# Kernel optimization log

Hardware: AMD Instinct MI355X
Metric: run time of the kernel (lower is better)

The kernel has to match this reference:

```python
import jax, jax.numpy as jnp
import numpy as np

BATCH = 16384
NUM_FEATURES = 1024  # sum(field_dims)
CROSS_DIMS = NUM_FEATURES * (NUM_FEATURES - 1) // 2  # 523776


def setup_inputs() -> dict:
    key = jax.random.key(0)
    kx, kw = jax.random.split(key)
    x = jax.random.uniform(kx, (BATCH, NUM_FEATURES), dtype=jnp.float32)
    # xavier-uniform init of a (cross_dims, 1) parameter: bound = sqrt(6/(fan_in+fan_out))
    bound = float(np.sqrt(6.0 / (CROSS_DIMS + 1)))
    w = jax.random.uniform(kw, (CROSS_DIMS,), dtype=jnp.float32, minval=-bound, maxval=bound)
    return {"x": x, "w": w}


def reference(x, w):
    # POLY2: out_b = sigmoid( sum_{i<j} w_{ij} * x_{b,i} * x_{b,j} )
    # sklearn PolynomialFeatures(interaction_only) emits pairs in combinations
    # (row-major i<j) order, identical to triu_indices(k=1) ordering.
    F = x.shape[1]
    iu, ju = jnp.triu_indices(F, k=1)
    W = jnp.zeros((F, F), dtype=x.dtype).at[iu, ju].set(w)  # [F,F] strictly upper-tri
    # quadratic form without materializing the [B, F*(F-1)/2] pairwise matrix
    out = jnp.einsum('bi,ij,bj->b', x, W, x)  # [B]
    return jax.nn.sigmoid(out.astype(jnp.float32))
```

## Files before the change

kernel.cpp:

```cpp
#include <hip/hip_runtime.h>
#include <hip/hip_bf16.h>

#define F 1024
#define B_ROWS 16384

typedef short v8s __attribute__((ext_vector_type(8)));
typedef float v4f __attribute__((ext_vector_type(4)));
typedef unsigned short v8u __attribute__((ext_vector_type(8)));
typedef unsigned short ushort_t;

__device__ __forceinline__ unsigned short f2bf(float f) {
    unsigned int u = __builtin_bit_cast(unsigned int, f);
    u = (u + 0x7FFFu + ((u >> 16) & 1u)) >> 16;
    return (unsigned short)u;
}

__device__ __forceinline__ void gload_lds16(const ushort_t* g, ushort_t* l) {
    __builtin_amdgcn_global_load_lds(
        (const __attribute__((address_space(1))) unsigned int*)g,
        (__attribute__((address_space(3))) unsigned int*)l,
        16, 0, 0);
}


__global__ __launch_bounds__(256) void prep_kernel(
        const float* __restrict__ w, const float* __restrict__ x,
        ushort_t* __restrict__ Bp, ushort_t* __restrict__ Xp,
        float* __restrict__ acc) {
    const int bid  = blockIdx.x;
    const int tid  = threadIdx.x;
    const int lane = tid & 63;
    const int wave = tid >> 6;
    const int l16  = lane & 15;
    const int quad = lane >> 4;

    if (bid < 64) {
        acc[bid * 256 + tid] = 0.0f;
    } else if (bid < 576) {
        const int c  = (bid - 64) * 4 + wave;
        const int n  = (c >> 5) * 16 + l16;
        const int k0 = (c & 31) * 32 + quad * 8;
        v8u o;
#pragma unroll
        for (int e = 0; e < 8; ++e) {
            const int k = k0 + e;
            float v = 0.0f;
            if (k < n) {
                const int idx = k * (F - 1) - (k * (k - 1)) / 2 + (n - k - 1);
                v = w[idx];
            }
            o[e] = f2bf(v);
        }
        *(v8u*)(Bp + (size_t)c * 512 + lane * 8) = o;
    } else {
        const int c  = (bid - 576) * 4 + wave;
        const int r  = (c >> 5) * 16 + l16;
        const int k0 = (c & 31) * 32 + quad * 8;
        const float* src = x + (size_t)r * F + k0;
        float4 v0 = *(const float4*)(src);
        float4 v1 = *(const float4*)(src + 4);
        v8u o;
        o[0] = f2bf(v0.x); o[1] = f2bf(v0.y); o[2] = f2bf(v0.z); o[3] = f2bf(v0.w);
        o[4] = f2bf(v1.x); o[5] = f2bf(v1.y); o[6] = f2bf(v1.z); o[7] = f2bf(v1.w);
        *(v8u*)(Xp + (size_t)c * 512 + lane * 8) = o;
    }
}

__global__ __launch_bounds__(256, 3) void gemm_kernel(
        const ushort_t* __restrict__ Xp,
        const ushort_t* __restrict__ Bp,
        const float*   __restrict__ Xf,
        float*         __restrict__ rowacc) {
    __shared__ ushort_t Bs[2 * 16 * 512];

    const int f   = blockIdx.x;
    const int xcd = f & 7;
    const int g   = f >> 3;
    const int y   = g & 15;
    const int nt  = 7 - (g >> 4);
    const int blockM = (xcd * 16 + y) * 128;
    const int blockN = nt * 128;
    const int nch    = 2 * (nt + 1);

    const int tid   = threadIdx.x;
    const int lane  = tid & 63;
    const int wave  = tid >> 6;
    const int waveM = wave >> 1;
    const int waveN = wave & 1;
    const int quad  = lane >> 4;
    const int l16   = lane & 15;

    const int mg = (blockM >> 4) + waveM * 4;
    const v8s* A8 = (const v8s*)Xp + (size_t)mg * 32 * 64 + lane;

    const int q0   = wave * 4;
    const int ngB  = nt * 8;

#define STAGE_B(c, buf)                                                        \
    {                                                                          \
        _Pragma("unroll")                                                      \
        for (int q = 0; q < 4; ++q) {                                          \
            const int qq  = q0 + q;                                            \
            const int kgl = qq >> 3, ngl = qq & 7;                             \
            gload_lds16(Bp + (size_t)((ngB + ngl) * 32 + (c) * 2 + kgl) * 512 + lane * 8, \
                        Bs + (buf) * 8192 + (kgl * 8 + ngl) * 512);            \
        }                                                                      \
    }

    v4f acc[4][4];
#pragma unroll
    for (int i = 0; i < 4; i++)
#pragma unroll
        for (int j = 0; j < 4; j++) acc[i][j] = (v4f)(0.0f);

    v8s a0[4], a1[4], bfr[4];

    STAGE_B(0, 0)
#pragma unroll
    for (int mi = 0; mi < 4; ++mi) a0[mi] = A8[(mi * 32 + 0) * 64];
    __syncthreads();

    for (int c = 0; c < nch; ++c) {
        const int  buf  = c & 1;
        const bool more = (c + 1 < nch);
        if (more) STAGE_B(c + 1, buf ^ 1)

#pragma unroll
        for (int ni = 0; ni < 4; ++ni)
            bfr[ni] = *(const v8s*)(Bs + buf * 8192 + (0 * 8 + waveN * 4 + ni) * 512 + lane * 8);
#pragma unroll
        for (int mi = 0; mi < 4; ++mi) a1[mi] = A8[(mi * 32 + 2 * c + 1) * 64];
#pragma unroll
        for (int mi = 0; mi < 4; ++mi)
#pragma unroll
            for (int ni = 0; ni < 4; ++ni)
                acc[mi][ni] = __builtin_amdgcn_mfma_f32_16x16x32_bf16(
                    a0[mi], bfr[ni], acc[mi][ni], 0, 0, 0);

#pragma unroll
        for (int ni = 0; ni < 4; ++ni)
            bfr[ni] = *(const v8s*)(Bs + buf * 8192 + (1 * 8 + waveN * 4 + ni) * 512 + lane * 8);
        if (more) {
#pragma unroll
            for (int mi = 0; mi < 4; ++mi) a0[mi] = A8[(mi * 32 + 2 * c + 2) * 64];
        }
#pragma unroll
        for (int mi = 0; mi < 4; ++mi)
#pragma unroll
            for (int ni = 0; ni < 4; ++ni)
                acc[mi][ni] = __builtin_amdgcn_mfma_f32_16x16x32_bf16(
                    a1[mi], bfr[ni], acc[mi][ni], 0, 0, 0);

        if (more) __syncthreads();
    }
#undef STAGE_B

#pragma unroll
    for (int mi = 0; mi < 4; mi++) {
#pragma unroll
        for (int r = 0; r < 4; r++) {
            const int b = blockM + waveM * 64 + mi * 16 + quad * 4 + r;
            const float* xr = Xf + (size_t)b * F + blockN + waveN * 64 + l16;
            float pv = acc[mi][0][r] * xr[0]
                     + acc[mi][1][r] * xr[16]
                     + acc[mi][2][r] * xr[32]
                     + acc[mi][3][r] * xr[48];
            pv += __shfl_xor(pv, 1);
            pv += __shfl_xor(pv, 2);
            pv += __shfl_xor(pv, 4);
            pv += __shfl_xor(pv, 8);
            if (l16 == 0) atomicAdd(&rowacc[b], pv);
        }
    }
}

__global__ void sigmoid_kernel(const float* __restrict__ acc, float* __restrict__ out) {
    int b = blockIdx.x * blockDim.x + threadIdx.x;
    out[b] = 1.0f / (1.0f + __expf(-acc[b]));
}

__global__ void fallback_kernel(const float* __restrict__ x, const float* __restrict__ w,
                                float* __restrict__ out) {
    __shared__ float xs[F];
    __shared__ float partial[4];
    const int b = blockIdx.x;
    for (int i = threadIdx.x; i < F; i += 256) xs[i] = x[(size_t)b * F + i];
    __syncthreads();
    float s = 0.0f;
    for (int i = threadIdx.x; i < F - 1; i += 256) {
        const float xi = xs[i];
        const int kbase = i * (F - 1) - (i * (i - 1)) / 2 - i - 1;
        for (int j = i + 1; j < F; j++) s += w[kbase + j] * xi * xs[j];
    }
    for (int off = 32; off; off >>= 1) s += __shfl_down(s, off);
    if ((threadIdx.x & 63) == 0) partial[threadIdx.x >> 6] = s;
    __syncthreads();
    if (threadIdx.x == 0) {
        float t = partial[0] + partial[1] + partial[2] + partial[3];
        out[b] = 1.0f / (1.0f + __expf(-t));
    }
}

extern "C" void kernel_launch(void* const* d_in, const int* in_sizes, int n_in,
                              void* d_out, int out_size, void* d_ws, size_t ws_size,
                              hipStream_t stream) {
    const float* x = (const float*)d_in[0];
    const float* w = (const float*)d_in[1];
    float* out = (float*)d_out;

    const size_t acc_bytes = 65536;
    const size_t B_bytes   = (size_t)F * F * 2;
    const size_t Xp_bytes  = (size_t)B_ROWS * F * 2;
    const size_t needed = acc_bytes + B_bytes + Xp_bytes;

    if (ws_size < needed) {
        fallback_kernel<<<B_ROWS, 256, 0, stream>>>(x, w, out);
        return;
    }

    float*    acc = (float*)d_ws;
    ushort_t* Bp  = (ushort_t*)((char*)d_ws + acc_bytes);
    ushort_t* Xp  = (ushort_t*)((char*)d_ws + acc_bytes + B_bytes);

    prep_kernel<<<64 + 512 + 8192, 256, 0, stream>>>(w, x, Bp, Xp, acc);
    gemm_kernel<<<1024, 256, 0, stream>>>(Xp, Bp, x, acc);
    sigmoid_kernel<<<B_ROWS / 256, 256, 0, stream>>>(acc, out);
}
```

Measured before the change: 133.2 us.

## Split heavy triangular N-tiles along K to balance GEMM block workloads

Measured after the change: 136.0 us. +2.1%, slower.

```diff
diff --git a/kernel.cpp b/kernel.cpp
--- a/kernel.cpp
+++ b/kernel.cpp
@@ -66,6 +66,10 @@
     }
 }
 
+#define NT_TBL 0x012454656737ULL
+#define C0_TBL 0x000560700800ULL
+#define NC_TBL 0x246565767888ULL
+
 __global__ __launch_bounds__(256, 3) void gemm_kernel(
         const ushort_t* __restrict__ Xp,
         const ushort_t* __restrict__ Bp,
@@ -75,12 +79,15 @@
 
     const int f   = blockIdx.x;
     const int xcd = f & 7;
-    const int g   = f >> 3;
-    const int y   = g & 15;
-    const int nt  = 7 - (g >> 4);
+    const int r   = f >> 3;
+    const int y   = r & 15;
+    const int j   = r >> 4;
+    const int nt  = (int)((NT_TBL >> (4 * j)) & 15);
+    const int c0  = (int)((C0_TBL >> (4 * j)) & 15);
+    const int nc  = (int)((NC_TBL >> (4 * j)) & 15);
     const int blockM = (xcd * 16 + y) * 128;
     const int blockN = nt * 128;
-    const int nch    = 2 * (nt + 1);
+    const int cEnd   = c0 + nc;
 
     const int tid   = threadIdx.x;
     const int lane  = tid & 63;
@@ -111,18 +118,18 @@
 #pragma unroll
     for (int i = 0; i < 4; i++)
 #pragma unroll
-        for (int j = 0; j < 4; j++) acc[i][j] = (v4f)(0.0f);
+        for (int j2 = 0; j2 < 4; j2++) acc[i][j2] = (v4f)(0.0f);
 
     v8s a0[4], a1[4], bfr[4];
 
-    STAGE_B(0, 0)
-#pragma unroll
-    for (int mi = 0; mi < 4; ++mi) a0[mi] = A8[(mi * 32 + 0) * 64];
+    STAGE_B(c0, 0)
+#pragma unroll
+    for (int mi = 0; mi < 4; ++mi) a0[mi] = A8[(mi * 32 + 2 * c0) * 64];
     __syncthreads();
 
-    for (int c = 0; c < nch; ++c) {
-        const int  buf  = c & 1;
-        const bool more = (c + 1 < nch);
+    for (int c = c0; c < cEnd; ++c) {
+        const int  buf  = (c - c0) & 1;
+        const bool more = (c + 1 < cEnd);
         if (more) STAGE_B(c + 1, buf ^ 1)
 
 #pragma unroll
@@ -158,13 +165,13 @@
 #pragma unroll
     for (int mi = 0; mi < 4; mi++) {
 #pragma unroll
-        for (int r = 0; r < 4; r++) {
-            const int b = blockM + waveM * 64 + mi * 16 + quad * 4 + r;
+        for (int rr = 0; rr < 4; rr++) {
+            const int b = blockM + waveM * 64 + mi * 16 + quad * 4 + rr;
             const float* xr = Xf + (size_t)b * F + blockN + waveN * 64 + l16;
-            float pv = acc[mi][0][r] * xr[0]
-                     + acc[mi][1][r] * xr[16]
-                     + acc[mi][2][r] * xr[32]
-                     + acc[mi][3][r] * xr[48];
+            float pv = acc[mi][0][rr] * xr[0]
+                     + acc[mi][1][rr] * xr[16]
+                     + acc[mi][2][rr] * xr[32]
+                     + acc[mi][3][rr] * xr[48];
             pv += __shfl_xor(pv, 1);
             pv += __shfl_xor(pv, 2);
             pv += __shfl_xor(pv, 4);
@@ -223,6 +230,6 @@
     ushort_t* Xp  = (ushort_t*)((char*)d_ws + acc_bytes + B_bytes);
 
     prep_kernel<<<64 + 512 + 8192, 256, 0, stream>>>(w, x, Bp, Xp, acc);
-    gemm_kernel<<<1024, 256, 0, stream>>>(Xp, Bp, x, acc);
+    gemm_kernel<<<1536, 256, 0, stream>>>(Xp, Bp, x, acc);
     sigmoid_kernel<<<B_ROWS / 256, 256, 0, stream>>>(acc, out);
 }
```

## Stage A tiles through LDS alongside B with half-depth k-steps

Applied to the files above, without the earlier changes.

Result: faster. 128.6 us (-3.4%).

```diff
diff --git a/kernel.cpp b/kernel.cpp
--- a/kernel.cpp
+++ b/kernel.cpp
@@ -71,7 +71,7 @@
         const ushort_t* __restrict__ Bp,
         const float*   __restrict__ Xf,
         float*         __restrict__ rowacc) {
-    __shared__ ushort_t Bs[2 * 16 * 512];
+    __shared__ ushort_t Ls[2 * 16 * 512];
 
     const int f   = blockIdx.x;
     const int xcd = f & 7;
@@ -80,7 +80,7 @@
     const int nt  = 7 - (g >> 4);
     const int blockM = (xcd * 16 + y) * 128;
     const int blockN = nt * 128;
-    const int nch    = 2 * (nt + 1);
+    const int tEnd   = 4 * (nt + 1);
 
     const int tid   = threadIdx.x;
     const int lane  = tid & 63;
@@ -90,20 +90,22 @@
     const int quad  = lane >> 4;
     const int l16   = lane & 15;
 
-    const int mg = (blockM >> 4) + waveM * 4;
-    const v8s* A8 = (const v8s*)Xp + (size_t)mg * 32 * 64 + lane;
-
-    const int q0   = wave * 4;
-    const int ngB  = nt * 8;
-
-#define STAGE_B(c, buf)                                                        \
+    const int mgBase = blockM >> 4;
+    const int ngB    = nt * 8;
+
+    const bool stageA = (wave < 2);
+    const int  qBase  = (wave & 1) * 4;
+    const ushort_t* gsrc0 = stageA
+        ? Xp + ((size_t)(mgBase + qBase) * 32) * 512
+        : Bp + ((size_t)(ngB  + qBase) * 32) * 512;
+    const int slot0 = (stageA ? 0 : 8) + qBase;
+
+#define STAGE(t, buf)                                                          \
     {                                                                          \
         _Pragma("unroll")                                                      \
         for (int q = 0; q < 4; ++q) {                                          \
-            const int qq  = q0 + q;                                            \
-            const int kgl = qq >> 3, ngl = qq & 7;                             \
-            gload_lds16(Bp + (size_t)((ngB + ngl) * 32 + (c) * 2 + kgl) * 512 + lane * 8, \
-                        Bs + (buf) * 8192 + (kgl * 8 + ngl) * 512);            \
+            gload_lds16(gsrc0 + ((size_t)q * 32 + (t)) * 512 + lane * 8,       \
+                        Ls + ((buf) * 16 + slot0 + q) * 512);                  \
         }                                                                      \
     }
 
@@ -113,47 +115,33 @@
 #pragma unroll
         for (int j = 0; j < 4; j++) acc[i][j] = (v4f)(0.0f);
 
-    v8s a0[4], a1[4], bfr[4];
-
-    STAGE_B(0, 0)
-#pragma unroll
-    for (int mi = 0; mi < 4; ++mi) a0[mi] = A8[(mi * 32 + 0) * 64];
+    v8s afr[4], bfr[4];
+
+    STAGE(0, 0)
     __syncthreads();
 
-    for (int c = 0; c < nch; ++c) {
-        const int  buf  = c & 1;
-        const bool more = (c + 1 < nch);
-        if (more) STAGE_B(c + 1, buf ^ 1)
-
+    for (int t = 0; t < tEnd; ++t) {
+        const int  buf  = t & 1;
+        const bool more = (t + 1 < tEnd);
+        if (more) STAGE(t + 1, buf ^ 1)
+
+#pragma unroll
+        for (int mi = 0; mi < 4; ++mi)
+            afr[mi] = *(const v8s*)(Ls + (buf * 16 + waveM * 4 + mi) * 512 + lane * 8);
 #pragma unroll
         for (int ni = 0; ni < 4; ++ni)
-            bfr[ni] = *(const v8s*)(Bs + buf * 8192 + (0 * 8 + waveN * 4 + ni) * 512 + lane * 8);
-#pragma unroll
-        for (int mi = 0; mi < 4; ++mi) a1[mi] = A8[(mi * 32 + 2 * c + 1) * 64];
+            bfr[ni] = *(const v8s*)(Ls + (buf * 16 + 8 + waveN * 4 + ni) * 512 + lane * 8);
+
 #pragma unroll
         for (int mi = 0; mi < 4; ++mi)
 #pragma unroll
             for (int ni = 0; ni < 4; ++ni)
                 acc[mi][ni] = __builtin_amdgcn_mfma_f32_16x16x32_bf16(
-                    a0[mi], bfr[ni], acc[mi][ni], 0, 0, 0);
-
-#pragma unroll
-        for (int ni = 0; ni < 4; ++ni)
-            bfr[ni] = *(const v8s*)(Bs + buf * 8192 + (1 * 8 + waveN * 4 + ni) * 512 + lane * 8);
-        if (more) {
-#pragma unroll
-            for (int mi = 0; mi < 4; ++mi) a0[mi] = A8[(mi * 32 + 2 * c + 2) * 64];
-        }
-#pragma unroll
-        for (int mi = 0; mi < 4; ++mi)
-#pragma unroll
-            for (int ni = 0; ni < 4; ++ni)
-                acc[mi][ni] = __builtin_amdgcn_mfma_f32_16x16x32_bf16(
-                    a1[mi], bfr[ni], acc[mi][ni], 0, 0, 0);
+                    afr[mi], bfr[ni], acc[mi][ni], 0, 0, 0);
 
         if (more) __syncthreads();
     }
-#undef STAGE_B
+#undef STAGE
 
 #pragma unroll
     for (int mi = 0; mi < 4; mi++) {
```
